# Performance work log

Hardware: AMD Instinct MI355X
Metric: run time of the kernel (lower is better)

The kernel has to match this reference:

```python
import jax, jax.numpy as jnp
import numpy as np

NEG = -10000.0
B, S, NL = 512, 1024, 49   # batch, seq_len, raw label count
L = NL + 2                  # label_size with <start>, <end>


def setup_inputs() -> dict:
    key = jax.random.key(0)
    k1, k2, k3, k4 = jax.random.split(key, 4)
    logits = jax.random.normal(k1, (B, S, NL), jnp.float32)
    transition = jax.random.normal(k2, (L, L), jnp.float32)
    # structural constraints from CRF.initialize(): nothing transitions into <end> row-wise,
    # nothing leaves <start> (transition[to, from] convention of the original code)
    transition = transition.at[:, L - 1].set(NEG).at[L - 2, :].set(NEG)
    labels = jax.random.randint(k3, (B, S), 0, NL, dtype=jnp.int32)
    lens = jax.random.randint(k4, (B,), 1, S + 1, dtype=jnp.int32)
    return {"logits": logits, "transition": transition, "labels": labels, "lens": lens}


def _seq_mask(lens, max_len):
    return jnp.arange(max_len)[None, :] < lens[:, None]


def _crf_loglik(logits, transition, labels, lens):
    b, s, nl = logits.shape
    l = transition.shape[0]
    start, end = l - 2, l - 1
    # pad_logits: append -10000 scores for <start>/<end>
    lg = jnp.concatenate([logits, jnp.full((b, s, 2), NEG, logits.dtype)], axis=2)  # [B,S,L]
    # ---- gold unary score ----
    unary = jnp.take_along_axis(lg, labels[:, :, None], axis=2)[..., 0]  # [B,S]
    unary = jnp.where(_seq_mask(lens, s), unary, 0.0).sum(axis=1)
    # ---- gold binary (transition) score ----
    ext = jnp.concatenate(
        [jnp.full((b, 1), start, labels.dtype), labels, jnp.full((b, 1), end, labels.dtype)], axis=1
    )  # [B,S+2]
    ext = jnp.where(_seq_mask(lens + 1, s + 2), ext, end)
    trn_scr = transition[ext[:, 1:], ext[:, :-1]]  # [B,S+1]; transition[to, from]
    binary = jnp.where(_seq_mask(lens + 1, s + 1), trn_scr, 0.0).sum(axis=1)
    gold = unary + binary
    # ---- partition function via forward-algorithm scan ----
    alpha0 = jnp.full((b, l), NEG, logits.dtype).at[:, start].set(0.0)
    def step(carry, logit_t):
        alpha, t = carry
        # mat[b,i,j] = logit_t[b,i] + alpha[b,j] + transition[i,j]
        mat = logit_t[:, :, None] + alpha[:, None, :] + transition[None, :, :]
        alpha_nxt = jax.scipy.special.logsumexp(mat, axis=2)
        alpha = jnp.where((t < lens)[:, None], alpha_nxt, alpha)
        return (alpha, t + 1), None
    (alpha, _), _ = jax.lax.scan(step, (alpha0, jnp.zeros((), lens.dtype)), jnp.swapaxes(lg, 0, 1))
    norm = jax.scipy.special.logsumexp(alpha + transition[end][None, :], axis=1)  # [B]
    return gold - norm


def reference(logits, transition, labels, lens):
    # CRF log-likelihood per sequence: gold path score minus log partition
    return _crf_loglik(logits, transition, labels, lens)
```

## Files before the change

### kernel.cpp

```cpp
#include <hip/hip_runtime.h>

#define NEGV (-10000.0f)

constexpr int B_ = 512;
constexpr int S_ = 1024;
constexpr int NL_ = 49;
constexpr int L_ = 51;

typedef __attribute__((ext_vector_type(4))) float f32x4;

__device__ __forceinline__ float readlane_f(float v, int l) {
    return __int_as_float(__builtin_amdgcn_readlane(__float_as_int(v), l));
}

template <int CTRL>
__device__ __forceinline__ float dpp_max_step(float v) {
    int sh = __builtin_amdgcn_update_dpp(__float_as_int(v), __float_as_int(v),
                                         CTRL, 0xf, 0xf, false);
    return fmaxf(v, __int_as_float(sh));
}

__device__ __forceinline__ float wave_max_sgpr(float v) {
    v = dpp_max_step<0x111>(v);
    v = dpp_max_step<0x112>(v);
    v = dpp_max_step<0x114>(v);
    v = dpp_max_step<0x118>(v);
    v = dpp_max_step<0x142>(v);
    v = dpp_max_step<0x143>(v);
    return readlane_f(v, 63);
}

__global__ __launch_bounds__(64, 1) void crf_fwd(
    const float* __restrict__ logits,
    const float* __restrict__ transition,
    const int*   __restrict__ labels,
    const int*   __restrict__ lens,
    float*       __restrict__ out)
{
    const int b    = blockIdx.x;
    const int lane = threadIdx.x;
    const int len  = __builtin_amdgcn_readfirstlane(lens[b]);

    const float* __restrict__ lg  = logits + (size_t)b * (S_ * NL_);
    const int*   __restrict__ lab = labels + (size_t)b * S_;

    __shared__ __align__(16) float pbuf[64];

    float Erow[NL_];
    float Tend, estart;
    {
        const bool st = (lane < NL_);
        const float* trow = transition + ((lane < L_) ? lane : 0) * L_;
        #pragma unroll
        for (int j = 0; j < NL_; ++j) {
            float tv = trow[j];
            Erow[j] = st ? __expf(tv) : 0.0f;
        }
        estart = __expf(trow[NL_]);
        Tend   = (lane < L_) ? transition[(L_ - 1) * L_ + lane] : NEGV;
    }

    float g = 0.0f;
    for (int t = lane; t < S_; t += 64) {
        if (t < len) {
            int c = lab[t];
            int p = (t == 0) ? (L_ - 2) : lab[t - 1];
            g += lg[t * NL_ + c] + transition[c * L_ + p];
            if (t == len - 1) g += transition[(L_ - 1) * L_ + c];
        }
    }
    #pragma unroll
    for (int o = 32; o >= 1; o >>= 1) g += __shfl_xor(g, o, 64);

    float P = 0.0f;
    if (lane < NL_) P = __expf(lg[lane]) * estart;
    pbuf[lane] = P;

    int   S = 0;
    int   kc;
    float scale_f;
    auto mk_scale = [&](float Mx) {
        int e = (__float_as_int(Mx) >> 23) & 255;
        if (e < 1) e = 1;
        kc      = e - 127;
        scale_f = __int_as_float((254 - e) << 23);
    };
    mk_scale(wave_max_sgpr(P));

    auto loadlg = [&](int t) -> float {
        float v = NEGV;
        if (lane < NL_) v = lg[t * NL_ + lane];
        return v;
    };

    float b0 = loadlg(1), b1 = loadlg(2), b2 = loadlg(3), b3 = loadlg(4);
    float b4 = loadlg(5), b5 = loadlg(6), b6 = loadlg(7), b7 = loadlg(8);

    auto substep = [&](float cur, int t) {
        float Mx = wave_max_sgpr(P);
        float d  = __expf(cur) * scale_f;
        const f32x4* pv = (const f32x4*)pbuf;
        f32x4 q0  = pv[0],  q1  = pv[1],  q2  = pv[2],  q3  = pv[3];
        f32x4 q4  = pv[4],  q5  = pv[5],  q6  = pv[6],  q7  = pv[7];
        f32x4 q8  = pv[8],  q9  = pv[9],  q10 = pv[10], q11 = pv[11];
        float p48 = pbuf[48];
        asm volatile(""
            : "+v"(q0), "+v"(q1), "+v"(q2),  "+v"(q3),
              "+v"(q4), "+v"(q5), "+v"(q6),  "+v"(q7),
              "+v"(q8), "+v"(q9), "+v"(q10), "+v"(q11), "+v"(p48));
        float y0 = 0.f, y1 = 0.f, y2 = 0.f, y3 = 0.f;
        #define FMA4(Q, base)                      \
            y0 = fmaf(Q.x, Erow[(base) + 0], y0);  \
            y1 = fmaf(Q.y, Erow[(base) + 1], y1);  \
            y2 = fmaf(Q.z, Erow[(base) + 2], y2);  \
            y3 = fmaf(Q.w, Erow[(base) + 3], y3);
        FMA4(q0,  0)  FMA4(q1,  4)  FMA4(q2,  8)  FMA4(q3, 12)
        FMA4(q4, 16)  FMA4(q5, 20)  FMA4(q6, 24)  FMA4(q7, 28)
        FMA4(q8, 32)  FMA4(q9, 36)  FMA4(q10, 40) FMA4(q11, 44)
        #undef FMA4
        float y  = (y0 + y1) + (y2 + y3);
        float Pn = d * y;
        pbuf[lane] = Pn;
        const bool live = (t < len);
        if (live && lane < NL_) P = Pn;
        if (live) S += kc;
        mk_scale(Mx);
    };

    const int tEnd = 1 + (((len - 1) + 7) & ~7);
    for (int t = 1; t < tEnd; t += 8) {
        int t8  = t + 8;  t8  = (t8  < S_) ? t8  : (S_ - 1);
        int t9  = t + 9;  t9  = (t9  < S_) ? t9  : (S_ - 1);
        int t10 = t + 10; t10 = (t10 < S_) ? t10 : (S_ - 1);
        int t11 = t + 11; t11 = (t11 < S_) ? t11 : (S_ - 1);
        int t12 = t + 12; t12 = (t12 < S_) ? t12 : (S_ - 1);
        int t13 = t + 13; t13 = (t13 < S_) ? t13 : (S_ - 1);
        int t14 = t + 14; t14 = (t14 < S_) ? t14 : (S_ - 1);
        int t15 = t + 15; t15 = (t15 < S_) ? t15 : (S_ - 1);
        substep(b0, t + 0); b0 = loadlg(t8);
        substep(b1, t + 1); b1 = loadlg(t9);
        substep(b2, t + 2); b2 = loadlg(t10);
        substep(b3, t + 3); b3 = loadlg(t11);
        substep(b4, t + 4); b4 = loadlg(t12);
        substep(b5, t + 5); b5 = loadlg(t13);
        substep(b6, t + 6); b6 = loadlg(t14);
        substep(b7, t + 7); b7 = loadlg(t15);
    }

    float alpha = logf(P) + (float)S * 0.69314718056f;

    float x = (lane < L_) ? (alpha + Tend) : NEGV;
    float mx = x;
    #pragma unroll
    for (int o = 32; o >= 1; o >>= 1) mx = fmaxf(mx, __shfl_xor(mx, o, 64));
    float e = __expf(x - mx);
    #pragma unroll
    for (int o = 32; o >= 1; o >>= 1) e += __shfl_xor(e, o, 64);
    float norm = mx + __logf(e);

    if (lane == 0) out[b] = g - norm;
}

extern "C" void kernel_launch(void* const* d_in, const int* in_sizes, int n_in,
                              void* d_out, int out_size, void* d_ws, size_t ws_size,
                              hipStream_t stream) {
    const float* logits     = (const float*)d_in[0];
    const float* transition = (const float*)d_in[1];
    const int*   labels     = (const int*)d_in[2];
    const int*   lens       = (const int*)d_in[3];
    float*       out        = (float*)d_out;
    crf_fwd<<<dim3(B_), dim3(64), 0, stream>>>(logits, transition, labels, lens, out);
}
```

Before: 462.0 us.

## Replace LDS broadcast matvec with DPP wave-rotate register matvec

The per-step 49x49 matrix-vector product no longer goes through shared memory. Each lane now keeps its alpha value in a register and rotates it across the wavefront with DPP wave_ror:1, while the exp(transition) row is stored pre-permuted per lane (64 registers). Two half-wave chains, one seeded by a shfl_xor by 32, are interleaved to shorten the dependency chain. The running-max reduction now reads the new P directly rather than the previous one. This removes the LDS write-then-read round trip on every timestep, at the cost of a longer serial chain of DPP moves (with possible hazard wait states), more FMAs and higher register pressure.

New measurement: 585.2 us. +26.7%, slower.

```diff
diff --git a/kernel.cpp b/kernel.cpp
--- a/kernel.cpp
+++ b/kernel.cpp
@@ -6,8 +6,6 @@
 constexpr int S_ = 1024;
 constexpr int NL_ = 49;
 constexpr int L_ = 51;
-
-typedef __attribute__((ext_vector_type(4))) float f32x4;
 
 __device__ __forceinline__ float readlane_f(float v, int l) {
     return __int_as_float(__builtin_amdgcn_readlane(__float_as_int(v), l));
@@ -30,6 +28,12 @@
     return readlane_f(v, 63);
 }
 
+__device__ __forceinline__ float dpp_ror1(float v) {
+    int iv = __float_as_int(v);
+    return __int_as_float(
+        __builtin_amdgcn_update_dpp(iv, iv, 0x13C, 0xf, 0xf, false));
+}
+
 __global__ __launch_bounds__(64, 1) void crf_fwd(
     const float* __restrict__ logits,
     const float* __restrict__ transition,
@@ -44,21 +48,16 @@
     const float* __restrict__ lg  = logits + (size_t)b * (S_ * NL_);
     const int*   __restrict__ lab = labels + (size_t)b * S_;
 
-    __shared__ __align__(16) float pbuf[64];
-
-    float Erow[NL_];
-    float Tend, estart;
-    {
-        const bool st = (lane < NL_);
-        const float* trow = transition + ((lane < L_) ? lane : 0) * L_;
-        #pragma unroll
-        for (int j = 0; j < NL_; ++j) {
-            float tv = trow[j];
-            Erow[j] = st ? __expf(tv) : 0.0f;
-        }
-        estart = __expf(trow[NL_]);
-        Tend   = (lane < L_) ? transition[(L_ - 1) * L_ + lane] : NEGV;
+    const float* trow = transition + ((lane < NL_) ? lane : 0) * L_;
+    float Eperm[64];
+    #pragma unroll
+    for (int s = 0; s < 64; ++s) {
+        int j = (lane - s) & 63;
+        float tv = trow[(j < NL_) ? j : 0];
+        Eperm[s] = (lane < NL_ && j < NL_) ? __expf(tv) : 0.0f;
     }
+    float estart = __expf(trow[NL_]);
+    float Tend   = (lane < L_) ? transition[(L_ - 1) * L_ + lane] : NEGV;
 
     float g = 0.0f;
     for (int t = lane; t < S_; t += 64) {
@@ -74,7 +73,6 @@
 
     float P = 0.0f;
     if (lane < NL_) P = __expf(lg[lane]) * estart;
-    pbuf[lane] = P;
 
     int   S = 0;
     int   kc;
@@ -97,34 +95,22 @@
     float b4 = loadlg(5), b5 = loadlg(6), b6 = loadlg(7), b7 = loadlg(8);
 
     auto substep = [&](float cur, int t) {
-        float Mx = wave_max_sgpr(P);
+        float rB = __shfl_xor(P, 32, 64);
         float d  = __expf(cur) * scale_f;
-        const f32x4* pv = (const f32x4*)pbuf;
-        f32x4 q0  = pv[0],  q1  = pv[1],  q2  = pv[2],  q3  = pv[3];
-        f32x4 q4  = pv[4],  q5  = pv[5],  q6  = pv[6],  q7  = pv[7];
-        f32x4 q8  = pv[8],  q9  = pv[9],  q10 = pv[10], q11 = pv[11];
-        float p48 = pbuf[48];
-        asm volatile(""
-            : "+v"(q0), "+v"(q1), "+v"(q2),  "+v"(q3),
-              "+v"(q4), "+v"(q5), "+v"(q6),  "+v"(q7),
-              "+v"(q8), "+v"(q9), "+v"(q10), "+v"(q11), "+v"(p48));
-        float y0 = 0.f, y1 = 0.f, y2 = 0.f, y3 = 0.f;
-        #define FMA4(Q, base)                      \
-            y0 = fmaf(Q.x, Erow[(base) + 0], y0);  \
-            y1 = fmaf(Q.y, Erow[(base) + 1], y1);  \
-            y2 = fmaf(Q.z, Erow[(base) + 2], y2);  \
-            y3 = fmaf(Q.w, Erow[(base) + 3], y3);
-        FMA4(q0,  0)  FMA4(q1,  4)  FMA4(q2,  8)  FMA4(q3, 12)
-        FMA4(q4, 16)  FMA4(q5, 20)  FMA4(q6, 24)  FMA4(q7, 28)
-        FMA4(q8, 32)  FMA4(q9, 36)  FMA4(q10, 40) FMA4(q11, 44)
-        #undef FMA4
-        float y  = (y0 + y1) + (y2 + y3);
+        float rA = P;
+        float yA0 = 0.f, yA1 = 0.f, yB0 = 0.f, yB1 = 0.f;
+        #pragma unroll
+        for (int s = 0; s < 32; s += 2) {
+            yA0 = fmaf(Eperm[s],      rA, yA0);  rA = dpp_ror1(rA);
+            yA1 = fmaf(Eperm[s + 1],  rA, yA1);  rA = dpp_ror1(rA);
+            yB0 = fmaf(Eperm[s + 32], rB, yB0);  rB = dpp_ror1(rB);
+            yB1 = fmaf(Eperm[s + 33], rB, yB1);  rB = dpp_ror1(rB);
+        }
+        float y  = (yA0 + yA1) + (yB0 + yB1);
         float Pn = d * y;
-        pbuf[lane] = Pn;
         const bool live = (t < len);
-        if (live && lane < NL_) P = Pn;
-        if (live) S += kc;
-        mk_scale(Mx);
+        if (live) { P = Pn; S += kc; }
+        mk_scale(wave_max_sgpr(Pn));
     };
 
     const int tEnd = 1 + (((len - 1) + 7) & ~7);
```
